# Performance work log

Measured on AMD Instinct MI355X. Metric: run time of the kernel, lower is better.

The kernel has to match this reference:

```python
import jax, jax.numpy as jnp
import numpy as np

B, SQ, SK, D, UNITS = 4, 2048, 2048, 1024, 1024

def setup_inputs() -> dict:
    key = jax.random.key(0)
    ks = jax.random.split(key, 5)
    scale = 1.0 / np.sqrt(D)
    return {
        "q": jax.random.normal(ks[0], (B, SQ, D), dtype=jnp.float32),
        "k": jax.random.normal(ks[1], (B, SK, D), dtype=jnp.float32),
        "v": jax.random.normal(ks[2], (B, SK, D), dtype=jnp.float32),
        "W1_w": jax.random.normal(ks[3], (D, UNITS), dtype=jnp.float32) * scale,
        "W1_b": jnp.zeros((UNITS,), dtype=jnp.float32),
        "W2_w": jax.random.normal(ks[4], (D, UNITS), dtype=jnp.float32) * scale,
        "W2_b": jnp.zeros((UNITS,), dtype=jnp.float32),
    }

def reference(q, k, v, W1_w, W1_b, W2_w, W2_b):
    # Dense projections (keras Dense: x @ W + b)
    l1 = q @ W1_w + W1_b            # [B, Sq, units]
    l2 = k @ W2_w + W2_b            # [B, Sk, units]
    # score = l1 @ l2^T, scaled by sqrt(score.shape[2]) == sqrt(Sk) (as in original)
    inv_scale = 1.0 / np.sqrt(k.shape[1]).astype(np.float32)
    score = jnp.einsum('bqu,bku->bqk', l1, l2) * inv_scale  # [B, Sq, Sk]
    dist = jax.nn.softmax(score, axis=-1)
    att = jnp.einsum('bqk,bkd->bqd', dist, v)               # [B, Sq, d_v]
    return att
```

## Files before the change

### kernel.cpp

```cpp
#include <hip/hip_runtime.h>
#include <cmath>
#include <stdint.h>


typedef short short8 __attribute__((ext_vector_type(8)));
typedef float f32x4 __attribute__((ext_vector_type(4)));
typedef __bf16 bf16x8 __attribute__((ext_vector_type(8)));

typedef __attribute__((address_space(3))) void lds_void;
typedef __attribute__((address_space(1))) void gbl_void;

__device__ __forceinline__ unsigned short f2b(float x) {
    unsigned u = __builtin_bit_cast(unsigned, x);
    u += 0x7fffu + ((u >> 16) & 1u);
    return (unsigned short)(u >> 16);
}

__global__ void prep_kernel(const float* __restrict__ q,
                            const float* __restrict__ k,
                            const float* __restrict__ v,
                            const float* __restrict__ W1,
                            const float* __restrict__ W2,
                            unsigned short* __restrict__ qbf,
                            unsigned short* __restrict__ kbf,
                            unsigned short* __restrict__ vT,
                            unsigned short* __restrict__ W1t,
                            unsigned short* __restrict__ W2t) {
    __shared__ float tile[32][33];
    const int bz = blockIdx.z;
    const int t = threadIdx.x;

    if (bz >= 6) {
        const float* in = (bz < 8) ? q : k;
        unsigned short* out = (bz < 8) ? qbf : kbf;
        const long zi = (bz - 6) & 1;
        const long fb = zi * 2048 + blockIdx.y * 64 + blockIdx.x;
        const long i = (fb * 256 + t) * 8;
        float4 a = *(const float4*)(in + i);
        float4 b = *(const float4*)(in + i + 4);
        union { short8 v8; unsigned short u[8]; } r;
        r.u[0] = f2b(a.x); r.u[1] = f2b(a.y); r.u[2] = f2b(a.z); r.u[3] = f2b(a.w);
        r.u[4] = f2b(b.x); r.u[5] = f2b(b.y); r.u[6] = f2b(b.z); r.u[7] = f2b(b.w);
        *(short8*)(out + i) = r.v8;
        return;
    }

    const float* in;
    unsigned short* out;
    int R, C;
    if (bz < 4) {
        R = 2048; C = 1024;
        in = v + (long)bz * R * C;
        out = vT + (long)bz * R * C;
    } else {
        R = 1024; C = 1024;
        if (blockIdx.x >= 32) return;
        in = (bz == 4) ? W1 : W2;
        out = (bz == 4) ? W1t : W2t;
    }
    const int rt = blockIdx.x * 32, ct = blockIdx.y * 32;
    {
        int r = t >> 3, c4 = (t & 7) * 4;
        float4 a = *(const float4*)(in + (long)(rt + r) * C + ct + c4);
        tile[r][c4 + 0] = a.x; tile[r][c4 + 1] = a.y;
        tile[r][c4 + 2] = a.z; tile[r][c4 + 3] = a.w;
    }
    __syncthreads();
    {
        int c = t >> 3, rg = (t & 7) * 4;
        ushort4 o;
        o.x = f2b(tile[rg + 0][c]); o.y = f2b(tile[rg + 1][c]);
        o.z = f2b(tile[rg + 2][c]); o.w = f2b(tile[rg + 3][c]);
        *(ushort4*)(out + (long)(ct + c) * R + rt + rg) = o;
    }
}

__device__ __forceinline__ void load16_to_lds(const unsigned short* g,
                                              unsigned short* l) {
    __builtin_amdgcn_global_load_lds((gbl_void*)g, (lds_void*)l, 16, 0, 0);
}

template <int MODE>
__global__ void gemm_bt_kernel(const unsigned short* __restrict__ A,
                               const unsigned short* __restrict__ Bt,
                               const float* __restrict__ bias0,
                               const float* __restrict__ bias1,
                               float* __restrict__ rowsum,
                               void* __restrict__ Cout,
                               int M, int N, int K,
                               float scale,
                               long sA, long sB, long sC) {
    __shared__ __align__(16) unsigned short As[128 * 64];
    __shared__ __align__(16) unsigned short Bs[128 * 64];

    int bx, by, bz;
    {
        const int nx = gridDim.x;
        const int Rt = gridDim.y * gridDim.z;
        if ((Rt & 7) == 0) {
            int flat = ((int)blockIdx.z * gridDim.y + blockIdx.y) * nx + blockIdx.x;
            int rpx = Rt >> 3;
            int c = flat & 7;
            int j = flat >> 3;
            bx = j / rpx;
            int yg = c * rpx + (j - bx * rpx);
            bz = yg / gridDim.y;
            by = yg - bz * gridDim.y;
        } else {
            bx = blockIdx.x; by = blockIdx.y; bz = blockIdx.z;
        }
    }

    A  += (long)bz * sA;
    Bt += (long)bz * sB;

    const int t = threadIdx.x;
    const int lane = t & 63;
    const int wave = t >> 6;
    const int wm = wave >> 1, wn = wave & 1;
    const int row0 = by * 128;
    const int col0 = bx * 128;

    const int rS = lane >> 3;
    const int kOffS = ((lane & 7) ^ rS) * 8;
    const unsigned short* gA[4];
    const unsigned short* gB[4];
    unsigned short* lA[4];
    unsigned short* lB[4];
#pragma unroll
    for (int i = 0; i < 4; i++) {
        const int rowl = i * 32 + wave * 8 + rS;
        const int ldsrow = i * 32 + wave * 8;
        gA[i] = A  + (long)(row0 + rowl) * K + kOffS;
        gB[i] = Bt + (long)(col0 + rowl) * K + kOffS;
        lA[i] = As + ldsrow * 64;
        lB[i] = Bs + ldsrow * 64;
    }

    const int lr = lane & 15;
    const int quad = lane >> 4;
    const int pc0 = (quad ^ (lr & 7)) * 8;
    const int pc1 = ((4 + quad) ^ (lr & 7)) * 8;

    f32x4 acc[4][4];
#pragma unroll
    for (int i = 0; i < 4; i++)
#pragma unroll
        for (int j = 0; j < 4; j++) acc[i][j] = f32x4{0.f, 0.f, 0.f, 0.f};

    for (int k0 = 0; k0 < K; k0 += 64) {
#pragma unroll
        for (int i = 0; i < 4; i++) {
            load16_to_lds(gA[i] + k0, lA[i]);
            load16_to_lds(gB[i] + k0, lB[i]);
        }
        __syncthreads();

#pragma unroll
        for (int ks = 0; ks < 2; ks++) {
            const int pc = ks ? pc1 : pc0;
            bf16x8 a[4], b[4];
#pragma unroll
            for (int i = 0; i < 4; i++) {
                a[i] = __builtin_bit_cast(bf16x8,
                    *(const short8*)(As + (wm * 64 + i * 16 + lr) * 64 + pc));
                b[i] = __builtin_bit_cast(bf16x8,
                    *(const short8*)(Bs + (wn * 64 + i * 16 + lr) * 64 + pc));
            }
#pragma unroll
            for (int i = 0; i < 4; i++)
#pragma unroll
                for (int j = 0; j < 4; j++)
                    acc[i][j] = __builtin_amdgcn_mfma_f32_16x16x32_bf16(
                        a[i], b[j], acc[i][j], 0, 0, 0);
        }
        __syncthreads();
    }

    const long cbase = (long)bz * sC;

    if (MODE == 0) {
        const float* bp = (bz && bias1) ? bias1 : bias0;
#pragma unroll
        for (int j = 0; j < 4; j++) {
            const int gcol = col0 + wn * 64 + j * 16 + lr;
            const float bv = bp[gcol];
#pragma unroll
            for (int i = 0; i < 4; i++) {
                const int growb = row0 + wm * 64 + i * 16 + quad * 4;
#pragma unroll
                for (int r = 0; r < 4; r++) {
                    float val = acc[i][j][r] * scale + bv;
                    ((unsigned short*)Cout)[cbase + (long)(growb + r) * N + gcol] = f2b(val);
                }
            }
        }
    } else if (MODE == 1) {
        float psum[4][4];
#pragma unroll
        for (int i = 0; i < 4; i++)
#pragma unroll
            for (int r = 0; r < 4; r++) psum[i][r] = 0.f;
#pragma unroll
        for (int j = 0; j < 4; j++) {
            const int gcol = col0 + wn * 64 + j * 16 + lr;
#pragma unroll
            for (int i = 0; i < 4; i++) {
                const int growb = row0 + wm * 64 + i * 16 + quad * 4;
#pragma unroll
                for (int r = 0; r < 4; r++) {
                    float e = __expf(acc[i][j][r] * scale);
                    psum[i][r] += e;
                    ((unsigned short*)Cout)[cbase + (long)(growb + r) * N + gcol] = f2b(e);
                }
            }
        }
#pragma unroll
        for (int i = 0; i < 4; i++)
#pragma unroll
            for (int r = 0; r < 4; r++) {
                float s = psum[i][r];
                s += __shfl_xor(s, 1);
                s += __shfl_xor(s, 2);
                s += __shfl_xor(s, 4);
                s += __shfl_xor(s, 8);
                if (lr == 0) {
                    const int grow = row0 + wm * 64 + i * 16 + quad * 4 + r;
                    atomicAdd(rowsum + (long)bz * M + grow, s);
                }
            }
    } else {
#pragma unroll
        for (int i = 0; i < 4; i++) {
            const int growb = row0 + wm * 64 + i * 16 + quad * 4;
#pragma unroll
            for (int r = 0; r < 4; r++) {
                const float inv = 1.0f / rowsum[(long)bz * M + growb + r];
#pragma unroll
                for (int j = 0; j < 4; j++) {
                    const int gcol = col0 + wn * 64 + j * 16 + lr;
                    ((float*)Cout)[cbase + (long)(growb + r) * N + gcol] =
                        acc[i][j][r] * inv;
                }
            }
        }
    }
}

extern "C" void kernel_launch(void* const* d_in, const int* in_sizes, int n_in,
                              void* d_out, int out_size, void* d_ws, size_t ws_size,
                              hipStream_t stream) {
    const float* q   = (const float*)d_in[0];
    const float* k   = (const float*)d_in[1];
    const float* v   = (const float*)d_in[2];
    const float* W1w = (const float*)d_in[3];
    const float* W1b = (const float*)d_in[4];
    const float* W2w = (const float*)d_in[5];
    const float* W2b = (const float*)d_in[6];
    float* out = (float*)d_out;

    const int B = 4, SQ = 2048, SK = 2048, D = 1024, U = 1024;
    char* ws = (char*)d_ws;
    const size_t MB = 1024 * 1024;
    unsigned short* qbf = (unsigned short*)(ws + 0);
    unsigned short* kbf = (unsigned short*)(ws + 16 * MB);
    unsigned short* vT  = (unsigned short*)(ws + 32 * MB);
    unsigned short* W1t = (unsigned short*)(ws + 48 * MB);
    unsigned short* W2t = (unsigned short*)(ws + 50 * MB);
    unsigned short* l1  = (unsigned short*)(ws + 52 * MB);
    unsigned short* l2  = (unsigned short*)(ws + 68 * MB);
    unsigned short* sc  = (unsigned short*)(ws + 0);
    float* rowsum = (float*)(ws + 50 * MB);

    prep_kernel<<<dim3(64, 32, 10), 256, 0, stream>>>(
        q, k, v, W1w, W2w, qbf, kbf, vT, W1t, W2t);
    gemm_bt_kernel<0><<<dim3(U / 128, (B * SQ) / 128, 2), 256, 0, stream>>>(
        qbf, W1t, W1b, W2b, nullptr, l1, B * SQ, U, D, 1.0f,
        (long)8 * 1024 * 1024, (long)1024 * 1024, (long)8 * 1024 * 1024);
    hipMemsetAsync(rowsum, 0, (size_t)B * SQ * sizeof(float), stream);
    const float invs = 1.0f / sqrtf((float)SK);
    gemm_bt_kernel<1><<<dim3(SK / 128, SQ / 128, B), 256, 0, stream>>>(
        l1, l2, nullptr, nullptr, rowsum, sc, SQ, SK, U, invs,
        (long)SQ * U, (long)SK * U, (long)SQ * SK);
    gemm_bt_kernel<2><<<dim3(D / 128, SQ / 128, B), 256, 0, stream>>>(
        sc, vT, nullptr, nullptr, rowsum, out, SQ, D, SK, 1.0f,
        (long)SQ * SK, (long)D * SK, (long)SQ * D);
}
```

Baseline: 273.5 us.

## Rewrite GEMM as 256x256 tile, 8-wave, double-buffered pipelined MFMA kernel

The bf16 GEMM kernel moves from 128x128 tiles with 4 waves and a single LDS buffer to 256x256 tiles with 8 waves. It double-buffers LDS in 32-wide k-halves, issuing async global-to-LDS loads ahead and staggering them across compute phases with manual vmcnt waits, barriers and setprio around the MFMA bursts. The aim is to hide global load latency behind matrix math and raise data reuse per tile. The cost is more registers and LDS per block, and fewer blocks per GEMM, which may leave CUs underused on the smaller grids.

Measured after the change: 288.4 us. 1.05x slower.

```diff
diff --git a/kernel.cpp b/kernel.cpp
--- a/kernel.cpp
+++ b/kernel.cpp
@@ -75,13 +75,66 @@
     }
 }
 
-__device__ __forceinline__ void load16_to_lds(const unsigned short* g,
-                                              unsigned short* l) {
-    __builtin_amdgcn_global_load_lds((gbl_void*)g, (lds_void*)l, 16, 0, 0);
-}
+
+#define BARRIER() do { asm volatile("" ::: "memory"); \
+    __builtin_amdgcn_s_barrier(); \
+    asm volatile("" ::: "memory"); } while (0)
+
+#define VMC6 asm volatile("s_waitcnt vmcnt(6)" ::: "memory")
+#define NOPSTMT do {} while (0)
+
+#define STG(P0, P1, LBASE, KO) do { \
+    const long ko_ = (KO); \
+    __builtin_amdgcn_global_load_lds((gbl_void*)((P0) + ko_), \
+        (lds_void*)((LBASE) + stgoff), 16, 0, 0); \
+    __builtin_amdgcn_global_load_lds((gbl_void*)((P1) + ko_), \
+        (lds_void*)((LBASE) + stgoff + 4096), 16, 0, 0); \
+} while (0)
+
+#define KOFF(T_, KH_) ((long)((((T_) < nTile) ? (T_) : ((T_) - nTile)) * 64 + (KH_) * 32))
+
+#define LDA_(BUF, KH, I_) __builtin_bit_cast(bf16x8, \
+    *(const short8*)(&As[BUF][KH][aoff + (I_) * 512]))
+#define LDB_(BUF, KH, J_) __builtin_bit_cast(bf16x8, \
+    *(const short8*)(&Bs[BUF][KH][boff + (J_) * 512]))
+
+#define MFMA_PAIR(JA, JB) do { \
+    _Pragma("unroll") \
+    for (int i_ = 0; i_ < 8; i_++) { \
+        acc[i_][JA] = __builtin_amdgcn_mfma_f32_16x16x32_bf16(a[i_], b[JA], acc[i_][JA], 0, 0, 0); \
+        acc[i_][JB] = __builtin_amdgcn_mfma_f32_16x16x32_bf16(a[i_], b[JB], acc[i_][JB], 0, 0, 0); \
+    } \
+} while (0)
+
+#define PHASE_A(BUF, KH, STAGE_STMT, TAIL_STMT) do { \
+    _Pragma("unroll") \
+    for (int i_ = 0; i_ < 8; i_++) a[i_] = LDA_(BUF, KH, i_); \
+    b[0] = LDB_(BUF, KH, 0); \
+    b[1] = LDB_(BUF, KH, 1); \
+    STAGE_STMT; \
+    BARRIER(); \
+    __builtin_amdgcn_s_setprio(1); \
+    MFMA_PAIR(0, 1); \
+    __builtin_amdgcn_s_setprio(0); \
+    TAIL_STMT; \
+    BARRIER(); \
+} while (0)
+
+#define PHASE_B(BUF, KH, STAGE_STMT, TAIL_STMT) do { \
+    b[2] = LDB_(BUF, KH, 2); \
+    b[3] = LDB_(BUF, KH, 3); \
+    STAGE_STMT; \
+    BARRIER(); \
+    __builtin_amdgcn_s_setprio(1); \
+    MFMA_PAIR(2, 3); \
+    __builtin_amdgcn_s_setprio(0); \
+    TAIL_STMT; \
+    BARRIER(); \
+} while (0)
 
 template <int MODE>
-__global__ void gemm_bt_kernel(const unsigned short* __restrict__ A,
+__global__ __launch_bounds__(512, 2) void gemm_bt_kernel(
+                               const unsigned short* __restrict__ A,
                                const unsigned short* __restrict__ Bt,
                                const float* __restrict__ bias0,
                                const float* __restrict__ bias1,
@@ -90,8 +143,8 @@
                                int M, int N, int K,
                                float scale,
                                long sA, long sB, long sC) {
-    __shared__ __align__(16) unsigned short As[128 * 64];
-    __shared__ __align__(16) unsigned short Bs[128 * 64];
+    __shared__ __align__(16) unsigned short As[2][2][8192];
+    __shared__ __align__(16) unsigned short Bs[2][2][8192];
 
     int bx, by, bz;
     {
@@ -114,68 +167,58 @@
     A  += (long)bz * sA;
     Bt += (long)bz * sB;
 
-    const int t = threadIdx.x;
-    const int lane = t & 63;
-    const int wave = t >> 6;
-    const int wm = wave >> 1, wn = wave & 1;
-    const int row0 = by * 128;
-    const int col0 = bx * 128;
-
-    const int rS = lane >> 3;
-    const int kOffS = ((lane & 7) ^ rS) * 8;
-    const unsigned short* gA[4];
-    const unsigned short* gB[4];
-    unsigned short* lA[4];
-    unsigned short* lB[4];
-#pragma unroll
-    for (int i = 0; i < 4; i++) {
-        const int rowl = i * 32 + wave * 8 + rS;
-        const int ldsrow = i * 32 + wave * 8;
-        gA[i] = A  + (long)(row0 + rowl) * K + kOffS;
-        gB[i] = Bt + (long)(col0 + rowl) * K + kOffS;
-        lA[i] = As + ldsrow * 64;
-        lB[i] = Bs + ldsrow * 64;
-    }
-
-    const int lr = lane & 15;
-    const int quad = lane >> 4;
-    const int pc0 = (quad ^ (lr & 7)) * 8;
-    const int pc1 = ((4 + quad) ^ (lr & 7)) * 8;
-
-    f32x4 acc[4][4];
-#pragma unroll
-    for (int i = 0; i < 4; i++)
+    const int tid = threadIdx.x;
+    const int lane = tid & 63;
+    const int w = tid >> 6;
+    const int wm = w >> 2, wn = w & 3;
+    const int row0 = by * 256;
+    const int col0 = bx * 256;
+
+    const int srow = lane >> 2;
+    const int sch  = (lane & 3) ^ ((lane >> 3) & 3);
+    const unsigned short* pA0 = A  + (long)(row0 + w * 16 + srow) * K + sch * 8;
+    const unsigned short* pA1 = pA0 + (long)128 * K;
+    const unsigned short* pB0 = Bt + (long)(col0 + w * 16 + srow) * K + sch * 8;
+    const unsigned short* pB1 = pB0 + (long)128 * K;
+    const int stgoff = w * 512;
+
+    const int lr = lane & 15, quad = lane >> 4;
+    const int rch  = (quad ^ ((lr >> 1) & 3)) * 8;
+    const int aoff = (wm * 128 + lr) * 32 + rch;
+    const int boff = (wn * 64  + lr) * 32 + rch;
+
+    const int nTile = K >> 6;
+    const int nIter = K >> 7;
+
+    f32x4 acc[8][4];
+#pragma unroll
+    for (int i = 0; i < 8; i++)
 #pragma unroll
         for (int j = 0; j < 4; j++) acc[i][j] = f32x4{0.f, 0.f, 0.f, 0.f};
-
-    for (int k0 = 0; k0 < K; k0 += 64) {
-#pragma unroll
-        for (int i = 0; i < 4; i++) {
-            load16_to_lds(gA[i] + k0, lA[i]);
-            load16_to_lds(gB[i] + k0, lB[i]);
-        }
-        __syncthreads();
-
-#pragma unroll
-        for (int ks = 0; ks < 2; ks++) {
-            const int pc = ks ? pc1 : pc0;
-            bf16x8 a[4], b[4];
-#pragma unroll
-            for (int i = 0; i < 4; i++) {
-                a[i] = __builtin_bit_cast(bf16x8,
-                    *(const short8*)(As + (wm * 64 + i * 16 + lr) * 64 + pc));
-                b[i] = __builtin_bit_cast(bf16x8,
-                    *(const short8*)(Bs + (wn * 64 + i * 16 + lr) * 64 + pc));
-            }
-#pragma unroll
-            for (int i = 0; i < 4; i++)
-#pragma unroll
-                for (int j = 0; j < 4; j++)
-                    acc[i][j] = __builtin_amdgcn_mfma_f32_16x16x32_bf16(
-                        a[i], b[j], acc[i][j], 0, 0, 0);
-        }
-        __syncthreads();
-    }
+    bf16x8 a[8], b[4];
+
+    STG(pA0, pA1, &As[0][0][0], KOFF(0, 0));
+    STG(pB0, pB1, &Bs[0][0][0], KOFF(0, 0));
+    STG(pA0, pA1, &As[0][1][0], KOFF(0, 1));
+    STG(pB0, pB1, &Bs[0][1][0], KOFF(0, 1));
+    STG(pA0, pA1, &As[1][0][0], KOFF(1, 0));
+    STG(pB0, pB1, &Bs[1][0][0], KOFF(1, 0));
+    STG(pA0, pA1, &As[1][1][0], KOFF(1, 1));
+    VMC6;
+    BARRIER();
+
+    for (int it = 0; it < nIter; ++it) {
+        const int t1 = 2 * it + 1, t2 = 2 * it + 2, t3 = 2 * it + 3;
+        PHASE_A(0, 0, STG(pB0, pB1, &Bs[1][1][0], KOFF(t1, 1)), NOPSTMT);
+        PHASE_B(0, 0, STG(pA0, pA1, &As[0][0][0], KOFF(t2, 0)), NOPSTMT);
+        PHASE_A(0, 1, STG(pB0, pB1, &Bs[0][0][0], KOFF(t2, 0)), NOPSTMT);
+        PHASE_B(0, 1, STG(pA0, pA1, &As[0][1][0], KOFF(t2, 1)), VMC6);
+        PHASE_A(1, 0, STG(pB0, pB1, &Bs[0][1][0], KOFF(t2, 1)), NOPSTMT);
+        PHASE_B(1, 0, STG(pA0, pA1, &As[1][0][0], KOFF(t3, 0)), NOPSTMT);
+        PHASE_A(1, 1, STG(pB0, pB1, &Bs[1][0][0], KOFF(t3, 0)), NOPSTMT);
+        PHASE_B(1, 1, STG(pA0, pA1, &As[1][1][0], KOFF(t3, 1)), VMC6);
+    }
+    asm volatile("s_waitcnt vmcnt(0)" ::: "memory");
 
     const long cbase = (long)bz * sC;
 
@@ -186,8 +229,8 @@
             const int gcol = col0 + wn * 64 + j * 16 + lr;
             const float bv = bp[gcol];
 #pragma unroll
-            for (int i = 0; i < 4; i++) {
-                const int growb = row0 + wm * 64 + i * 16 + quad * 4;
+            for (int i = 0; i < 8; i++) {
+                const int growb = row0 + wm * 128 + i * 16 + quad * 4;
 #pragma unroll
                 for (int r = 0; r < 4; r++) {
                     float val = acc[i][j][r] * scale + bv;
@@ -196,17 +239,17 @@
             }
         }
     } else if (MODE == 1) {
-        float psum[4][4];
-#pragma unroll
-        for (int i = 0; i < 4; i++)
+        float psum[8][4];
+#pragma unroll
+        for (int i = 0; i < 8; i++)
 #pragma unroll
             for (int r = 0; r < 4; r++) psum[i][r] = 0.f;
 #pragma unroll
         for (int j = 0; j < 4; j++) {
             const int gcol = col0 + wn * 64 + j * 16 + lr;
 #pragma unroll
-            for (int i = 0; i < 4; i++) {
-                const int growb = row0 + wm * 64 + i * 16 + quad * 4;
+            for (int i = 0; i < 8; i++) {
+                const int growb = row0 + wm * 128 + i * 16 + quad * 4;
 #pragma unroll
                 for (int r = 0; r < 4; r++) {
                     float e = __expf(acc[i][j][r] * scale);
@@ -216,7 +259,7 @@
             }
         }
 #pragma unroll
-        for (int i = 0; i < 4; i++)
+        for (int i = 0; i < 8; i++)
 #pragma unroll
             for (int r = 0; r < 4; r++) {
                 float s = psum[i][r];
@@ -225,14 +268,14 @@
                 s += __shfl_xor(s, 4);
                 s += __shfl_xor(s, 8);
                 if (lr == 0) {
-                    const int grow = row0 + wm * 64 + i * 16 + quad * 4 + r;
+                    const int grow = row0 + wm * 128 + i * 16 + quad * 4 + r;
                     atomicAdd(rowsum + (long)bz * M + grow, s);
                 }
             }
     } else {
 #pragma unroll
-        for (int i = 0; i < 4; i++) {
-            const int growb = row0 + wm * 64 + i * 16 + quad * 4;
+        for (int i = 0; i < 8; i++) {
+            const int growb = row0 + wm * 128 + i * 16 + quad * 4;
 #pragma unroll
             for (int r = 0; r < 4; r++) {
                 const float inv = 1.0f / rowsum[(long)bz * M + growb + r];
@@ -274,15 +317,15 @@
 
     prep_kernel<<<dim3(64, 32, 10), 256, 0, stream>>>(
         q, k, v, W1w, W2w, qbf, kbf, vT, W1t, W2t);
-    gemm_bt_kernel<0><<<dim3(U / 128, (B * SQ) / 128, 2), 256, 0, stream>>>(
+    gemm_bt_kernel<0><<<dim3(U / 256, (B * SQ) / 256, 2), 512, 0, stream>>>(
         qbf, W1t, W1b, W2b, nullptr, l1, B * SQ, U, D, 1.0f,
         (long)8 * 1024 * 1024, (long)1024 * 1024, (long)8 * 1024 * 1024);
     hipMemsetAsync(rowsum, 0, (size_t)B * SQ * sizeof(float), stream);
     const float invs = 1.0f / sqrtf((float)SK);
-    gemm_bt_kernel<1><<<dim3(SK / 128, SQ / 128, B), 256, 0, stream>>>(
+    gemm_bt_kernel<1><<<dim3(SK / 256, SQ / 256, B), 512, 0, stream>>>(
         l1, l2, nullptr, nullptr, rowsum, sc, SQ, SK, U, invs,
         (long)SQ * U, (long)SK * U, (long)SQ * SK);
-    gemm_bt_kernel<2><<<dim3(D / 128, SQ / 128, B), 256, 0, stream>>>(
+    gemm_bt_kernel<2><<<dim3(D / 256, SQ / 256, B), 512, 0, stream>>>(
         sc, vT, nullptr, nullptr, rowsum, out, SQ, D, SK, 1.0f,
         (long)SQ * SK, (long)D * SK, (long)SQ * D);
 }
```

## Add 256x128 tile GEMM with 512 threads for projection and score stages

Applied to the files above, without the earlier changes.

Introduces a new GEMM kernel that uses 256-row by 128-column output tiles with 8 waves per block. The two projection GEMMs and the score GEMM move to it, while the final attention-times-V GEMM keeps the 128x128 kernel. The larger tile reuses each B tile across twice as many rows, cutting global/L2 traffic per FLOP. The trade-off is more LDS per block, fewer blocks in the grid, and possible occupancy or register-pressure limits. The main loop is still single-buffered with two syncs per k-step.

Result: faster. 267.4 us (-2.2%).

```diff
diff --git a/kernel.cpp b/kernel.cpp
--- a/kernel.cpp
+++ b/kernel.cpp
@@ -81,7 +81,8 @@
 }
 
 template <int MODE>
-__global__ void gemm_bt_kernel(const unsigned short* __restrict__ A,
+__global__ __launch_bounds__(512, 4) void gemm256_kernel(
+                               const unsigned short* __restrict__ A,
                                const unsigned short* __restrict__ Bt,
                                const float* __restrict__ bias0,
                                const float* __restrict__ bias1,
@@ -90,7 +91,7 @@
                                int M, int N, int K,
                                float scale,
                                long sA, long sB, long sC) {
-    __shared__ __align__(16) unsigned short As[128 * 64];
+    __shared__ __align__(16) unsigned short As[256 * 64];
     __shared__ __align__(16) unsigned short Bs[128 * 64];
 
     int bx, by, bz;
@@ -118,6 +119,175 @@
     const int lane = t & 63;
     const int wave = t >> 6;
     const int wm = wave >> 1, wn = wave & 1;
+    const int row0 = by * 256;
+    const int col0 = bx * 128;
+
+    const int rS = lane >> 3;
+    const int kOffS = ((lane & 7) ^ rS) * 8;
+    const unsigned short* gA[4];
+    unsigned short* lA[4];
+    const unsigned short* gB[2];
+    unsigned short* lB[2];
+#pragma unroll
+    for (int i = 0; i < 4; i++) {
+        const int rowl = wave * 32 + i * 8;
+        gA[i] = A + (long)(row0 + rowl + rS) * K + kOffS;
+        lA[i] = As + rowl * 64;
+    }
+#pragma unroll
+    for (int i = 0; i < 2; i++) {
+        const int rowl = wave * 16 + i * 8;
+        gB[i] = Bt + (long)(col0 + rowl + rS) * K + kOffS;
+        lB[i] = Bs + rowl * 64;
+    }
+
+    const int lr = lane & 15;
+    const int quad = lane >> 4;
+    const int pc0 = (quad ^ (lr & 7)) * 8;
+    const int pc1 = ((4 + quad) ^ (lr & 7)) * 8;
+
+    f32x4 acc[4][4];
+#pragma unroll
+    for (int i = 0; i < 4; i++)
+#pragma unroll
+        for (int j = 0; j < 4; j++) acc[i][j] = f32x4{0.f, 0.f, 0.f, 0.f};
+
+    for (int k0 = 0; k0 < K; k0 += 64) {
+#pragma unroll
+        for (int i = 0; i < 4; i++) load16_to_lds(gA[i] + k0, lA[i]);
+#pragma unroll
+        for (int i = 0; i < 2; i++) load16_to_lds(gB[i] + k0, lB[i]);
+        __syncthreads();
+
+#pragma unroll
+        for (int ks = 0; ks < 2; ks++) {
+            const int pc = ks ? pc1 : pc0;
+            bf16x8 a[4], b[4];
+#pragma unroll
+            for (int i = 0; i < 4; i++) {
+                a[i] = __builtin_bit_cast(bf16x8,
+                    *(const short8*)(As + (wm * 64 + i * 16 + lr) * 64 + pc));
+                b[i] = __builtin_bit_cast(bf16x8,
+                    *(const short8*)(Bs + (wn * 64 + i * 16 + lr) * 64 + pc));
+            }
+#pragma unroll
+            for (int i = 0; i < 4; i++)
+#pragma unroll
+                for (int j = 0; j < 4; j++)
+                    acc[i][j] = __builtin_amdgcn_mfma_f32_16x16x32_bf16(
+                        a[i], b[j], acc[i][j], 0, 0, 0);
+        }
+        __syncthreads();
+    }
+
+    const long cbase = (long)bz * sC;
+
+    if (MODE == 0) {
+        const float* bp = (bz && bias1) ? bias1 : bias0;
+#pragma unroll
+        for (int j = 0; j < 4; j++) {
+            const int gcol = col0 + wn * 64 + j * 16 + lr;
+            const float bv = bp[gcol];
+#pragma unroll
+            for (int i = 0; i < 4; i++) {
+                const int growb = row0 + wm * 64 + i * 16 + quad * 4;
+#pragma unroll
+                for (int r = 0; r < 4; r++) {
+                    float val = acc[i][j][r] * scale + bv;
+                    ((unsigned short*)Cout)[cbase + (long)(growb + r) * N + gcol] = f2b(val);
+                }
+            }
+        }
+    } else if (MODE == 1) {
+        float psum[4][4];
+#pragma unroll
+        for (int i = 0; i < 4; i++)
+#pragma unroll
+            for (int r = 0; r < 4; r++) psum[i][r] = 0.f;
+#pragma unroll
+        for (int j = 0; j < 4; j++) {
+            const int gcol = col0 + wn * 64 + j * 16 + lr;
+#pragma unroll
+            for (int i = 0; i < 4; i++) {
+                const int growb = row0 + wm * 64 + i * 16 + quad * 4;
+#pragma unroll
+                for (int r = 0; r < 4; r++) {
+                    float e = __expf(acc[i][j][r] * scale);
+                    psum[i][r] += e;
+                    ((unsigned short*)Cout)[cbase + (long)(growb + r) * N + gcol] = f2b(e);
+                }
+            }
+        }
+#pragma unroll
+        for (int i = 0; i < 4; i++)
+#pragma unroll
+            for (int r = 0; r < 4; r++) {
+                float s = psum[i][r];
+                s += __shfl_xor(s, 1);
+                s += __shfl_xor(s, 2);
+                s += __shfl_xor(s, 4);
+                s += __shfl_xor(s, 8);
+                if (lr == 0) {
+                    const int grow = row0 + wm * 64 + i * 16 + quad * 4 + r;
+                    atomicAdd(rowsum + (long)bz * M + grow, s);
+                }
+            }
+    } else {
+#pragma unroll
+        for (int i = 0; i < 4; i++) {
+            const int growb = row0 + wm * 64 + i * 16 + quad * 4;
+#pragma unroll
+            for (int r = 0; r < 4; r++) {
+                const float inv = 1.0f / rowsum[(long)bz * M + growb + r];
+#pragma unroll
+                for (int j = 0; j < 4; j++) {
+                    const int gcol = col0 + wn * 64 + j * 16 + lr;
+                    ((float*)Cout)[cbase + (long)(growb + r) * N + gcol] =
+                        acc[i][j][r] * inv;
+                }
+            }
+        }
+    }
+}
+
+template <int MODE>
+__global__ void gemm128_kernel(const unsigned short* __restrict__ A,
+                               const unsigned short* __restrict__ Bt,
+                               const float* __restrict__ bias0,
+                               const float* __restrict__ bias1,
+                               float* __restrict__ rowsum,
+                               void* __restrict__ Cout,
+                               int M, int N, int K,
+                               float scale,
+                               long sA, long sB, long sC) {
+    __shared__ __align__(16) unsigned short As[128 * 64];
+    __shared__ __align__(16) unsigned short Bs[128 * 64];
+
+    int bx, by, bz;
+    {
+        const int nx = gridDim.x;
+        const int Rt = gridDim.y * gridDim.z;
+        if ((Rt & 7) == 0) {
+            int flat = ((int)blockIdx.z * gridDim.y + blockIdx.y) * nx + blockIdx.x;
+            int rpx = Rt >> 3;
+            int c = flat & 7;
+            int j = flat >> 3;
+            bx = j / rpx;
+            int yg = c * rpx + (j - bx * rpx);
+            bz = yg / gridDim.y;
+            by = yg - bz * gridDim.y;
+        } else {
+            bx = blockIdx.x; by = blockIdx.y; bz = blockIdx.z;
+        }
+    }
+
+    A  += (long)bz * sA;
+    Bt += (long)bz * sB;
+
+    const int t = threadIdx.x;
+    const int lane = t & 63;
+    const int wave = t >> 6;
+    const int wm = wave >> 1, wn = wave & 1;
     const int row0 = by * 128;
     const int col0 = bx * 128;
 
@@ -274,15 +444,15 @@
 
     prep_kernel<<<dim3(64, 32, 10), 256, 0, stream>>>(
         q, k, v, W1w, W2w, qbf, kbf, vT, W1t, W2t);
-    gemm_bt_kernel<0><<<dim3(U / 128, (B * SQ) / 128, 2), 256, 0, stream>>>(
+    gemm256_kernel<0><<<dim3(U / 128, (B * SQ) / 256, 2), 512, 0, stream>>>(
         qbf, W1t, W1b, W2b, nullptr, l1, B * SQ, U, D, 1.0f,
         (long)8 * 1024 * 1024, (long)1024 * 1024, (long)8 * 1024 * 1024);
     hipMemsetAsync(rowsum, 0, (size_t)B * SQ * sizeof(float), stream);
     const float invs = 1.0f / sqrtf((float)SK);
-    gemm_bt_kernel<1><<<dim3(SK / 128, SQ / 128, B), 256, 0, stream>>>(
+    gemm256_kernel<1><<<dim3(SK / 128, SQ / 256, B), 512, 0, stream>>>(
         l1, l2, nullptr, nullptr, rowsum, sc, SQ, SK, U, invs,
         (long)SQ * U, (long)SK * U, (long)SQ * SK);
-    gemm_bt_kernel<2><<<dim3(D / 128, SQ / 128, B), 256, 0, stream>>>(
+    gemm128_kernel<2><<<dim3(D / 128, SQ / 128, B), 256, 0, stream>>>(
         sc, vT, nullptr, nullptr, rowsum, out, SQ, D, SK, 1.0f,
         (long)SQ * SK, (long)D * SK, (long)SQ * D);
 }
```
